# Kernel optimization log

Measured on AMD Instinct MI355X. Metric: run time of the kernel, lower is better.

Reference implementation:

```python
import jax, jax.numpy as jnp
import numpy as np

B, NM, NA, D = 16, 4000, 128, 128  # scenes, map nodes/scene, agents/scene, feature dim
DIST_TH = 7.0
BOX = 100.0


def _gn(x, g, b, eps=1e-5):
    # GroupNorm with 1 group over [N, C]: per-row normalization, biased variance, affine.
    mu = jnp.mean(x, axis=-1, keepdims=True)
    var = jnp.mean((x - mu) ** 2, axis=-1, keepdims=True)
    return (x - mu) * jax.lax.rsqrt(var + eps) * g + b


def _forward(feat, turn, control, intersect, agents, map_ctrs, agent_ctrs,
             meta_w, meta_g, meta_b,
             dist_w1, dist_b1, dist_w2, dist_g2, dist_b2,
             query_w, query_g, query_b,
             ctx_w1, ctx_g1, ctx_b1, ctx_w2,
             agt_w, norm_g, norm_b,
             lin_w, lin_g, lin_b,
             hi, wi):
    relu = jax.nn.relu
    # meta fuse: cat(feat, turn, control, intersect) -> Linear(n_map+4 -> n_map) + GN + ReLU
    x = jnp.concatenate([feat, turn, control[:, None], intersect[:, None]], axis=1)
    x = relu(_gn(x @ meta_w.T, meta_g, meta_b))
    for i in range(2):  # two Att layers with distinct weights
        res = x
        d = map_ctrs[hi] - agent_ctrs[wi]                         # [E, 2]
        d = relu(d @ dist_w1[i].T + dist_b1[i])                   # [E, D]
        d = relu(_gn(d @ dist_w2[i].T, dist_g2[i], dist_b2[i]))
        q = relu(_gn(x[hi] @ query_w[i].T, query_g[i], query_b[i]))
        c = jnp.concatenate([d, q, agents[wi]], axis=1)           # [E, 3D]
        c = relu(_gn(c @ ctx_w1[i].T, ctx_g1[i], ctx_b1[i]))
        c = c @ ctx_w2[i].T                                       # [E, D]
        x = x @ agt_w[i].T                                        # [N, D]
        x = x.at[hi].add(c)                                       # index_add_ scatter
        x = relu(_gn(x, norm_g[i], norm_b[i]))
        x = _gn(x @ lin_w[i].T, lin_g[i], lin_b[i])               # Linear act=False
        x = relu(x + res)
    return x


def setup_inputs() -> dict:
    # edge list (hi: map node, wi: agent) built exactly like Att's per-scene dist<=th nonzero
    rng = np.random.default_rng(0)
    mc = rng.uniform(0.0, BOX, (B, NM, 2)).astype(np.float32)
    ac = rng.uniform(0.0, BOX, (B, NA, 2)).astype(np.float32)
    dist = np.sqrt(((mc[:, :, None, :] - ac[:, None, :, :]) ** 2).sum(-1))
    bb, h, w = np.nonzero(dist <= DIST_TH)
    hi = jnp.asarray((bb * NM + h).astype(np.int32))
    wi = jnp.asarray((bb * NA + w).astype(np.int32))

    key = jax.random.key(0)
    ks = jax.random.split(key, 20)
    s = 0.02
    nrm = lambda k, shape: jax.random.normal(k, shape, jnp.float32) * s
    return {
        "feat": jax.random.normal(ks[0], (B * NM, D), jnp.float32),
        "turn": jax.random.normal(ks[1], (B * NM, 2), jnp.float32),
        "control": jax.random.uniform(ks[2], (B * NM,), jnp.float32),
        "intersect": jax.random.uniform(ks[3], (B * NM,), jnp.float32),
        "agents": jax.random.normal(ks[4], (B * NA, D), jnp.float32),
        "map_ctrs": jnp.asarray(mc.reshape(-1, 2)),
        "agent_ctrs": jnp.asarray(ac.reshape(-1, 2)),
        "meta_w": nrm(ks[5], (D, D + 4)),
        "meta_g": jnp.ones((D,), jnp.float32),
        "meta_b": jnp.zeros((D,), jnp.float32),
        "dist_w1": nrm(ks[6], (2, D, 2)),
        "dist_b1": nrm(ks[7], (2, D)),
        "dist_w2": nrm(ks[8], (2, D, D)),
        "dist_g2": jnp.ones((2, D), jnp.float32),
        "dist_b2": jnp.zeros((2, D), jnp.float32),
        "query_w": nrm(ks[9], (2, D, D)),
        "query_g": jnp.ones((2, D), jnp.float32),
        "query_b": jnp.zeros((2, D), jnp.float32),
        "ctx_w1": nrm(ks[10], (2, D, 3 * D)),
        "ctx_g1": jnp.ones((2, D), jnp.float32),
        "ctx_b1": jnp.zeros((2, D), jnp.float32),
        "ctx_w2": nrm(ks[11], (2, D, D)),
        "agt_w": nrm(ks[12], (2, D, D)),
        "norm_g": jnp.ones((2, D), jnp.float32),
        "norm_b": jnp.zeros((2, D), jnp.float32),
        "lin_w": nrm(ks[13], (2, D, D)),
        "lin_g": jnp.ones((2, D), jnp.float32),
        "lin_b": jnp.zeros((2, D), jnp.float32),
        "hi": hi,
        "wi": wi,
    }


def reference(feat, turn, control, intersect, agents, map_ctrs, agent_ctrs,
              meta_w, meta_g, meta_b,
              dist_w1, dist_b1, dist_w2, dist_g2, dist_b2,
              query_w, query_g, query_b,
              ctx_w1, ctx_g1, ctx_b1, ctx_w2,
              agt_w, norm_g, norm_b,
              lin_w, lin_g, lin_b,
              hi, wi):
    return _forward(feat, turn, control, intersect, agents, map_ctrs, agent_ctrs,
                    meta_w, meta_g, meta_b,
                    dist_w1, dist_b1, dist_w2, dist_g2, dist_b2,
                    query_w, query_g, query_b,
                    ctx_w1, ctx_g1, ctx_b1, ctx_w2,
                    agt_w, norm_g, norm_b,
                    lin_w, lin_g, lin_b,
                    hi, wi)
```

## Files before the change

kernel.cpp:

```cpp
#include <hip/hip_runtime.h>


typedef __attribute__((ext_vector_type(8))) short short8v;
typedef __attribute__((ext_vector_type(4))) float f32x4;

#define NXCD 8

__device__ __forceinline__ unsigned short f2b(float f) {
    union { float f; unsigned u; } v; v.f = f;
    return (unsigned short)((v.u + 0x7fffu + ((v.u >> 16) & 1u)) >> 16);
}
__device__ __forceinline__ unsigned pk2(float a, float b) {
    return (unsigned)f2b(a) | ((unsigned)f2b(b) << 16);
}
__device__ __forceinline__ float bflo(unsigned u) { return __uint_as_float(u << 16); }
__device__ __forceinline__ float bfhi(unsigned u) { return __uint_as_float(u & 0xffff0000u); }

union U4S8 { unsigned u[4]; short8v v; };

__device__ __forceinline__ void bar_lds() {
    __builtin_amdgcn_sched_barrier(0);
    asm volatile("s_waitcnt lgkmcnt(0)" ::: "memory");
    __builtin_amdgcn_s_barrier();
    __builtin_amdgcn_sched_barrier(0);
}

template<int NV>
__device__ __forceinline__ void sload(short8v (&v)[NV], const unsigned short* __restrict__ src,
                                      int t) {
#pragma unroll
    for (int i = 0; i < NV; i++) v[i] = *(const short8v*)(src + (size_t)i * 2048 + t * 8);
}
template<int NV>
__device__ __forceinline__ void swrite(unsigned short* dst, const short8v (&v)[NV], int t) {
#pragma unroll
    for (int i = 0; i < NV; i++) *(short8v*)(dst + i * 2048 + t * 8) = v[i];
}

template<int NK>
__device__ __forceinline__ void wgemm_lds(const unsigned short* Wlds,
                                          const short8v* bf, f32x4 (&acc)[8], int l) {
#pragma unroll
    for (int mt = 0; mt < 8; mt++) {
        acc[mt] = (f32x4){0.f, 0.f, 0.f, 0.f};
#pragma unroll
        for (int kk = 0; kk < NK; kk++) {
            const short8v a = *(const short8v*)(Wlds + ((mt * NK + kk) * 64 + l) * 8);
            acc[mt] = __builtin_amdgcn_mfma_f32_16x16x32_bf16(a, bf[kk], acc[mt], 0, 0, 0);
        }
    }
}

__device__ __forceinline__ void gn_apply8(f32x4 (&acc)[8], const float* __restrict__ g,
                                          const float* __restrict__ b, int lg, bool relu) {
    float s = 0.f, s2 = 0.f;
#pragma unroll
    for (int mt = 0; mt < 8; mt++)
#pragma unroll
        for (int q = 0; q < 4; q++) { const float v = acc[mt][q]; s += v; s2 += v * v; }
    s += __shfl_xor(s, 16, 64); s2 += __shfl_xor(s2, 16, 64);
    s += __shfl_xor(s, 32, 64); s2 += __shfl_xor(s2, 32, 64);
    const float mu = s * (1.f / 128.f);
    const float rs = rsqrtf(s2 * (1.f / 128.f) - mu * mu + 1e-5f);
#pragma unroll
    for (int mt = 0; mt < 8; mt++) {
        const f32x4 g4 = *(const f32x4*)(g + mt * 16 + lg * 4);
        const f32x4 b4 = *(const f32x4*)(b + mt * 16 + lg * 4);
#pragma unroll
        for (int q = 0; q < 4; q++) {
            float y = (acc[mt][q] - mu) * rs * g4[q] + b4[q];
            acc[mt][q] = relu ? fmaxf(y, 0.f) : y;
        }
    }
}

__device__ __forceinline__ void pack_p(const f32x4 (&acc)[8], unsigned (&p)[8][2]) {
#pragma unroll
    for (int mt = 0; mt < 8; mt++) {
        p[mt][0] = pk2(acc[mt][0], acc[mt][1]);
        p[mt][1] = pk2(acc[mt][2], acc[mt][3]);
    }
}

__device__ __forceinline__ void lds_put(unsigned short* wslice, const unsigned (&p)[8][2],
                                        int lg, int col) {
#pragma unroll
    for (int mt = 0; mt < 8; mt++) {
        const unsigned long long v = (unsigned long long)p[mt][0] |
                                     ((unsigned long long)p[mt][1] << 32);
        *(unsigned long long*)((char*)wslice + ((col * 256 + mt * 32 + lg * 8) ^ ((col & 7) << 4))) = v;
    }
}
__device__ __forceinline__ void lds_wait() {
    asm volatile("s_waitcnt lgkmcnt(0)" ::: "memory");
    __builtin_amdgcn_sched_barrier(0);
}
__device__ __forceinline__ void lds_get(const unsigned short* wslice, int lg, int col,
                                        short8v* bf) {
#pragma unroll
    for (int kk = 0; kk < 4; kk++)
        bf[kk] = *(const short8v*)((const char*)wslice +
                 ((col * 256 + kk * 64 + lg * 16) ^ ((col & 7) << 4)));
}
__device__ __forceinline__ void relayout1(unsigned short* wslice, int lg, int col,
                                          f32x4 (&acc)[8], short8v* bf) {
    unsigned p[8][2];
    pack_p(acc, p); lds_put(wslice, p, lg, col); lds_wait(); lds_get(wslice, lg, col, bf);
}

__device__ __forceinline__ void load_bfrag_row(const float* __restrict__ src, int lg,
                                               short8v* bf) {
#pragma unroll
    for (int kk = 0; kk < 4; kk++) {
        const f32x4 a = *(const f32x4*)(src + kk * 32 + lg * 8);
        const f32x4 b = *(const f32x4*)(src + kk * 32 + lg * 8 + 4);
        U4S8 u;
        u.u[0] = pk2(a[0], a[1]); u.u[1] = pk2(a[2], a[3]);
        u.u[2] = pk2(b[0], b[1]); u.u[3] = pk2(b[2], b[3]);
        bf[kk] = u.v;
    }
}
__device__ __forceinline__ void store_rows(float* dst, const f32x4 (&acc)[8], int lg) {
#pragma unroll
    for (int mt = 0; mt < 8; mt++) *(f32x4*)(dst + mt * 16 + lg * 4) = acc[mt];
}
__device__ __forceinline__ void store_rows_bf16(unsigned short* dst, const f32x4 (&acc)[8], int lg) {
#pragma unroll
    for (int mt = 0; mt < 8; mt++) {
        uint2 u; u.x = pk2(acc[mt][0], acc[mt][1]); u.y = pk2(acc[mt][2], acc[mt][3]);
        *(uint2*)(dst + mt * 16 + lg * 4) = u;
    }
}
__device__ __forceinline__ void residual_add_bf16(f32x4 (&acc)[8],
                                                  const unsigned short* __restrict__ rp,
                                                  int lg, bool relu) {
#pragma unroll
    for (int mt = 0; mt < 8; mt++) {
        const uint2 u = *(const uint2*)(rp + mt * 16 + lg * 4);
        acc[mt][0] += bflo(u.x); acc[mt][1] += bfhi(u.x);
        acc[mt][2] += bflo(u.y); acc[mt][3] += bfhi(u.y);
        if (relu) {
#pragma unroll
            for (int q = 0; q < 4; q++) acc[mt][q] = fmaxf(acc[mt][q], 0.f);
        }
    }
}
__device__ __forceinline__ void gather_issue(const unsigned short* __restrict__ Qc,
                                             const unsigned short* __restrict__ Acp,
                                             int h, int w, int lg,
                                             uint2 (&qv)[8], uint2 (&av)[8]) {
    const int hl = (h < 0) ? 0 : h;
    const unsigned short* qp = Qc  + (size_t)hl * 128 + lg * 4;
    const unsigned short* ap = Acp + (size_t)w  * 128 + lg * 4;
#pragma unroll
    for (int mt = 0; mt < 8; mt++) {
        qv[mt] = *(const uint2*)(qp + mt * 16);
        av[mt] = *(const uint2*)(ap + mt * 16);
    }
}
__device__ __forceinline__ void gather_add(f32x4 (&acc)[8], const uint2 (&qv)[8],
                                           const uint2 (&av)[8]) {
#pragma unroll
    for (int mt = 0; mt < 8; mt++) {
        acc[mt][0] += bflo(qv[mt].x) + bflo(av[mt].x);
        acc[mt][1] += bfhi(qv[mt].x) + bfhi(av[mt].x);
        acc[mt][2] += bflo(qv[mt].y) + bflo(av[mt].y);
        acc[mt][3] += bfhi(qv[mt].y) + bfhi(av[mt].y);
    }
}
__device__ __forceinline__ void build_d1(const float* __restrict__ dw1,
                                         const float* __restrict__ db1,
                                         float dx, float dy, int lg, short8v* bf) {
#pragma unroll
    for (int kk = 0; kk < 4; kk++) {
        U4S8 u;
#pragma unroll
        for (int ii = 0; ii < 4; ii++) {
            const int c0 = kk * 32 + lg * 8 + ii * 2;
            const float2 wa = *(const float2*)(dw1 + 2 * c0);
            const float2 wb = *(const float2*)(dw1 + 2 * c0 + 2);
            const float2 bb = *(const float2*)(db1 + c0);
            u.u[ii] = pk2(fmaxf(fmaf(wa.x, dx, fmaf(wa.y, dy, bb.x)), 0.f),
                          fmaxf(fmaf(wb.x, dx, fmaf(wb.y, dy, bb.y)), 0.f));
        }
        bf[kk] = u.v;
    }
}

struct PrepJob { const float* src; int dst; int ld; int kmax; int nk; };
struct PrepJobs { PrepJob j[17]; };

__global__ __launch_bounds__(64) void prep_weights(PrepJobs P, unsigned short* __restrict__ pool) {
    const PrepJob J = P.j[blockIdx.y];
    const int f = blockIdx.x;
    if (f >= 8 * J.nk) return;
    const int l = threadIdx.x;
    const int n = (f / J.nk) * 16 + (l & 15);
    const int kb = (f % J.nk) * 32 + (l >> 4) * 8;
    float v[8];
#pragma unroll
    for (int i = 0; i < 8; i++) {
        const int k = kb + i;
        v[i] = (k < J.kmax) ? J.src[(size_t)n * J.ld + k] : 0.f;
    }
    U4S8 u;
#pragma unroll
    for (int i = 0; i < 4; i++) u.u[i] = pk2(v[2 * i], v[2 * i + 1]);
    *(short8v*)(pool + J.dst + ((size_t)f * 64 + l) * 8) = u.v;
}

__device__ __forceinline__ void agent_path(
    unsigned short* Wlds, int abid, int NA, const float* __restrict__ agents,
    const unsigned short* __restrict__ Wc1a, unsigned short* Ac,
    int t, int wid, int l, int lg, int col)
{
    short8v sv[8];
    sload<8>(sv, Wc1a, t);
    const int r = abid * 64 + wid * 16 + col;
    const int rc = min(r, NA - 1);
    short8v bf[4];
    load_bfrag_row(agents + (size_t)rc * 128, lg, bf);
    swrite<8>(Wlds, sv, t);
    bar_lds();
    f32x4 acc[8];
    wgemm_lds<4>(Wlds, bf, acc, l);
    if (r < NA) store_rows_bf16(Ac + (size_t)r * 128, acc, lg);
}

__global__ __launch_bounds__(256, 2) void meta_node(
    const int N, const int NA, const int gN,
    const float* __restrict__ feat, const float* __restrict__ turn,
    const float* __restrict__ ctrl, const float* __restrict__ inter,
    const float* __restrict__ agents,
    const unsigned short* __restrict__ Wm,
    const float* __restrict__ mg, const float* __restrict__ mb,
    const unsigned short* __restrict__ Wagt, const unsigned short* __restrict__ Wq,
    const float* __restrict__ qg, const float* __restrict__ qb,
    const unsigned short* __restrict__ Wc1q, const unsigned short* __restrict__ Wc1a,
    unsigned short* __restrict__ xA, float* __restrict__ xB,
    unsigned short* __restrict__ Qc, unsigned short* __restrict__ Ac)
{
    __shared__ unsigned short Wlds[20480];
    const int t = threadIdx.x, wid = t >> 6, l = t & 63, lg = l >> 4, col = l & 15;
    unsigned short* wslice = Wlds + wid * 2048;
    if (blockIdx.x >= gN) {
        agent_path(Wlds, blockIdx.x - gN, NA, agents, Wc1a, Ac, t, wid, l, lg, col);
        return;
    }
    const int r = blockIdx.x * 64 + wid * 16 + col;
    const int rc = min(r, N - 1);

    short8v s10[10];
    sload<10>(s10, Wm, t);
    short8v bf[5];
    load_bfrag_row(feat + (size_t)rc * 128, lg, bf);
    {
        U4S8 u; u.u[0] = 0; u.u[1] = 0; u.u[2] = 0; u.u[3] = 0;
        if (lg == 0) {
            const float2 tv = *(const float2*)(turn + (size_t)rc * 2);
            u.u[0] = pk2(tv.x, tv.y);
            u.u[1] = pk2(ctrl[rc], inter[rc]);
        }
        bf[4] = u.v;
    }
    swrite<10>(Wlds, s10, t);
    bar_lds();

    short8v s8[8];
    sload<8>(s8, Wagt, t);
    f32x4 acc[8];
    wgemm_lds<5>(Wlds, bf, acc, l);
    gn_apply8(acc, mg, mb, lg, true);
    if (r < N) store_rows_bf16(xA + (size_t)r * 128, acc, lg);
    bar_lds();
    short8v bx[4];
    relayout1(wslice, lg, col, acc, bx);
    bar_lds();
    swrite<8>(Wlds, s8, t);
    bar_lds();

    sload<8>(s8, Wq, t);
    wgemm_lds<4>(Wlds, bx, acc, l);
    if (r < N) store_rows(xB + (size_t)r * 128, acc, lg);
    bar_lds();
    swrite<8>(Wlds, s8, t);
    bar_lds();

    sload<8>(s8, Wc1q, t);
    wgemm_lds<4>(Wlds, bx, acc, l);
    gn_apply8(acc, qg, qb, lg, true);
    bar_lds();
    relayout1(wslice, lg, col, acc, bx);
    bar_lds();
    swrite<8>(Wlds, s8, t);
    bar_lds();

    wgemm_lds<4>(Wlds, bx, acc, l);
    if (r < N) store_rows_bf16(Qc + (size_t)r * 128, acc, lg);
}

__device__ __forceinline__ void post_load_gn(const float* xp,
                                             const float* __restrict__ ng,
                                             const float* __restrict__ nb,
                                             int lg, short8v* bf) {
    float v[4][8];
    float s = 0.f, s2 = 0.f;
#pragma unroll
    for (int kk = 0; kk < 4; kk++) {
        *(f32x4*)(v[kk])     = *(const f32x4*)(xp + kk * 32 + lg * 8);
        *(f32x4*)(v[kk] + 4) = *(const f32x4*)(xp + kk * 32 + lg * 8 + 4);
#pragma unroll
        for (int i = 0; i < 8; i++) { s += v[kk][i]; s2 += v[kk][i] * v[kk][i]; }
    }
    s += __shfl_xor(s, 16, 64); s2 += __shfl_xor(s2, 16, 64);
    s += __shfl_xor(s, 32, 64); s2 += __shfl_xor(s2, 32, 64);
    const float mu = s * (1.f / 128.f);
    const float rs = rsqrtf(s2 * (1.f / 128.f) - mu * mu + 1e-5f);
#pragma unroll
    for (int kk = 0; kk < 4; kk++) {
        float y[8];
#pragma unroll
        for (int i = 0; i < 8; i += 4) {
            const f32x4 g4 = *(const f32x4*)(ng + kk * 32 + lg * 8 + i);
            const f32x4 b4 = *(const f32x4*)(nb + kk * 32 + lg * 8 + i);
#pragma unroll
            for (int q = 0; q < 4; q++)
                y[i + q] = fmaxf((v[kk][i + q] - mu) * rs * g4[q] + b4[q], 0.f);
        }
        U4S8 u;
#pragma unroll
        for (int i = 0; i < 4; i++) u.u[i] = pk2(y[2 * i], y[2 * i + 1]);
        bf[kk] = u.v;
    }
}

__global__ __launch_bounds__(256, 2) void post_node(
    const int N, const int NA, const int gN,
    const float* __restrict__ ng, const float* __restrict__ nb,
    const unsigned short* __restrict__ Wlin,
    const float* __restrict__ lgam, const float* __restrict__ lbet,
    const float* __restrict__ agents, const unsigned short* __restrict__ Wc1a,
    const unsigned short* __restrict__ Wagt, const unsigned short* __restrict__ Wq,
    const float* __restrict__ qg, const float* __restrict__ qb,
    const unsigned short* __restrict__ Wc1q,
    unsigned short* xA, float* xB,
    unsigned short* __restrict__ Qc, unsigned short* __restrict__ Ac)
{
    __shared__ unsigned short Wlds[16384];
    const int t = threadIdx.x, wid = t >> 6, l = t & 63, lg = l >> 4, col = l & 15;
    unsigned short* wslice = Wlds + wid * 2048;
    if (blockIdx.x >= gN) {
        agent_path(Wlds, blockIdx.x - gN, NA, agents, Wc1a, Ac, t, wid, l, lg, col);
        return;
    }
    const int r = blockIdx.x * 64 + wid * 16 + col;
    const int rc = min(r, N - 1);

    short8v s8[8];
    sload<8>(s8, Wlin, t);
    short8v bf[4];
    post_load_gn(xB + (size_t)rc * 128, ng, nb, lg, bf);
    swrite<8>(Wlds, s8, t);
    bar_lds();

    sload<8>(s8, Wagt, t);
    f32x4 acc[8];
    wgemm_lds<4>(Wlds, bf, acc, l);
    gn_apply8(acc, lgam, lbet, lg, false);
    residual_add_bf16(acc, xA + (size_t)rc * 128, lg, true);
    if (r < N) store_rows_bf16(xA + (size_t)r * 128, acc, lg);
    bar_lds();
    short8v bx[4];
    relayout1(wslice, lg, col, acc, bx);
    bar_lds();
    swrite<8>(Wlds, s8, t);
    bar_lds();

    sload<8>(s8, Wq, t);
    wgemm_lds<4>(Wlds, bx, acc, l);
    if (r < N) store_rows(xB + (size_t)r * 128, acc, lg);
    bar_lds();
    swrite<8>(Wlds, s8, t);
    bar_lds();

    sload<8>(s8, Wc1q, t);
    wgemm_lds<4>(Wlds, bx, acc, l);
    gn_apply8(acc, qg, qb, lg, true);
    bar_lds();
    relayout1(wslice, lg, col, acc, bx);
    bar_lds();
    swrite<8>(Wlds, s8, t);
    bar_lds();

    wgemm_lds<4>(Wlds, bx, acc, l);
    if (r < N) store_rows_bf16(Qc + (size_t)r * 128, acc, lg);
}

__global__ __launch_bounds__(256, 2) void post_final(
    const int N,
    const float* __restrict__ xB,
    const float* __restrict__ ng, const float* __restrict__ nb,
    const unsigned short* __restrict__ Wlin,
    const float* __restrict__ lgam, const float* __restrict__ lbet,
    const unsigned short* __restrict__ res, float* __restrict__ out)
{
    __shared__ unsigned short Wlds[16384];
    const int t = threadIdx.x, wid = t >> 6, l = t & 63, lg = l >> 4, col = l & 15;
    const int r = blockIdx.x * 64 + wid * 16 + col;
    const int rc = min(r, N - 1);
    short8v s8[8];
    sload<8>(s8, Wlin, t);
    short8v bf[4];
    post_load_gn(xB + (size_t)rc * 128, ng, nb, lg, bf);
    swrite<8>(Wlds, s8, t);
    bar_lds();
    f32x4 acc[8];
    wgemm_lds<4>(Wlds, bf, acc, l);
    gn_apply8(acc, lgam, lbet, lg, false);
    residual_add_bf16(acc, res + (size_t)rc * 128, lg, true);
    if (r < N) store_rows(out + (size_t)r * 128, acc, lg);
}

__global__ __launch_bounds__(256, 2) void edge_mfma(
    const int E, const int nwg,
    const int* __restrict__ hi, const int* __restrict__ wi,
    const float* __restrict__ mc, const float* __restrict__ ac,
    const float* __restrict__ dw1, const float* __restrict__ db1,
    const unsigned short* __restrict__ Wd2, const float* __restrict__ dg2, const float* __restrict__ db2,
    const unsigned short* __restrict__ Wc1d, const float* __restrict__ cg1, const float* __restrict__ cb1,
    const unsigned short* __restrict__ Wc2,
    const unsigned short* __restrict__ Qc, const unsigned short* __restrict__ Acp,
    float* __restrict__ OUT)
{
    __shared__ unsigned short Wlds[16384];
    __shared__ int s_h[64];
    const int t = threadIdx.x, wid = t >> 6, l = t & 63, lg = l >> 4, col = l & 15;
    unsigned short* wslice = Wlds + wid * 2048;

    int bid;
    {
        const int orig = blockIdx.x;
        const int q = nwg / NXCD, r = nwg % NXCD;
        const int xcd = orig % NXCD, i = orig / NXCD;
        bid = (xcd < r ? xcd * (q + 1) : r * (q + 1) + (xcd - r) * q) + i;
    }
    const int eidx = bid * 64 + wid * 16 + col;

    short8v s8[8];
    sload<8>(s8, Wd2, t);

    int h = -1, w = 0;
    if (eidx < E) { h = hi[eidx]; w = wi[eidx]; }
    if (lg == 0) s_h[wid * 16 + col] = h;
    const int hl = (h < 0) ? 0 : h;
    const float2 mcv = *(const float2*)(mc + 2 * (size_t)hl);
    const float2 acv = *(const float2*)(ac + 2 * (size_t)w);
    const float dx = mcv.x - acv.x, dy = mcv.y - acv.y;

    uint2 qv[8], av[8];
    gather_issue(Qc, Acp, h, w, lg, qv, av);

    short8v bf[4];
    build_d1(dw1, db1, dx, dy, lg, bf);

    swrite<8>(Wlds, s8, t);
    bar_lds();

    sload<8>(s8, Wc1d, t);
    f32x4 acc[8];
    wgemm_lds<4>(Wlds, bf, acc, l);
    gn_apply8(acc, dg2, db2, lg, true);
    bar_lds();
    relayout1(wslice, lg, col, acc, bf);
    bar_lds();
    swrite<8>(Wlds, s8, t);
    bar_lds();

    sload<8>(s8, Wc2, t);
    wgemm_lds<4>(Wlds, bf, acc, l);
    gather_add(acc, qv, av);
    gn_apply8(acc, cg1, cb1, lg, true);
    bar_lds();
    relayout1(wslice, lg, col, acc, bf);
    bar_lds();
    swrite<8>(Wlds, s8, t);
    bar_lds();

    wgemm_lds<4>(Wlds, bf, acc, l);
    bar_lds();
    unsigned p[8][2];
    pack_p(acc, p); lds_put(wslice, p, lg, col); lds_wait();

#pragma unroll
    for (int pass = 0; pass < 2; pass++) {
        const int c = pass * 64 + l;
        float pend = 0.f; int ph = -1;
#pragma unroll
        for (int e = 0; e < 16; e++) {
            const int he = s_h[wid * 16 + e];
            const unsigned short uv = *(const unsigned short*)((const char*)wslice +
                                      ((e * 256 + c * 2) ^ ((e & 7) << 4)));
            const float v = __uint_as_float((unsigned)uv << 16);
            if (he == ph) pend += v;
            else {
                if (ph >= 0) atomicAdd(&OUT[(size_t)ph * 128 + c], pend);
                ph = he; pend = v;
            }
        }
        if (ph >= 0) atomicAdd(&OUT[(size_t)ph * 128 + c], pend);
    }
}

extern "C" void kernel_launch(void* const* d_in, const int* in_sizes, int n_in,
                              void* d_out, int out_size, void* d_ws, size_t ws_size,
                              hipStream_t stream)
{
    const float* feat    = (const float*)d_in[0];
    const float* turn    = (const float*)d_in[1];
    const float* ctrl    = (const float*)d_in[2];
    const float* inter   = (const float*)d_in[3];
    const float* agents  = (const float*)d_in[4];
    const float* mc      = (const float*)d_in[5];
    const float* ac      = (const float*)d_in[6];
    const float* meta_w  = (const float*)d_in[7];
    const float* meta_g  = (const float*)d_in[8];
    const float* meta_b  = (const float*)d_in[9];
    const float* dist_w1 = (const float*)d_in[10];
    const float* dist_b1 = (const float*)d_in[11];
    const float* dist_w2 = (const float*)d_in[12];
    const float* dist_g2 = (const float*)d_in[13];
    const float* dist_b2 = (const float*)d_in[14];
    const float* query_w = (const float*)d_in[15];
    const float* query_g = (const float*)d_in[16];
    const float* query_b = (const float*)d_in[17];
    const float* ctx_w1  = (const float*)d_in[18];
    const float* ctx_g1  = (const float*)d_in[19];
    const float* ctx_b1  = (const float*)d_in[20];
    const float* ctx_w2  = (const float*)d_in[21];
    const float* agt_w   = (const float*)d_in[22];
    const float* norm_g  = (const float*)d_in[23];
    const float* norm_b  = (const float*)d_in[24];
    const float* lin_w   = (const float*)d_in[25];
    const float* lin_g   = (const float*)d_in[26];
    const float* lin_b   = (const float*)d_in[27];
    const int*   hi      = (const int*)d_in[28];
    const int*   wi      = (const int*)d_in[29];

    const int E  = in_sizes[28];
    const int N  = in_sizes[0] / 128;
    const int NA = in_sizes[4] / 128;

    unsigned short* xA = (unsigned short*)d_ws;
    float* xB = (float*)(xA + (size_t)N * 128);
    unsigned short* pool = (unsigned short*)(xB + (size_t)N * 128);

    const int FR128  = 8 * 4 * 64 * 8;
    const int FRMETA = 8 * 5 * 64 * 8;
    const int POOL_ELEMS = FRMETA + 16 * FR128;

    unsigned short* Ac = pool + POOL_ELEMS;
    unsigned short* Qc = (unsigned short*)d_out;

    PrepJobs P;
    P.j[0] = { meta_w, 0, 132, 132, 5 };
    for (int i = 0; i < 2; i++) {
        const int b = FRMETA + i * 8 * FR128;
        P.j[1 + i * 8 + 0] = { query_w + (size_t)i * 16384, b + 0 * FR128, 128, 128, 4 };
        P.j[1 + i * 8 + 1] = { agt_w   + (size_t)i * 16384, b + 1 * FR128, 128, 128, 4 };
        P.j[1 + i * 8 + 2] = { dist_w2 + (size_t)i * 16384, b + 2 * FR128, 128, 128, 4 };
        P.j[1 + i * 8 + 3] = { ctx_w1  + (size_t)i * 49152,       b + 3 * FR128, 384, 128, 4 };
        P.j[1 + i * 8 + 4] = { ctx_w1  + (size_t)i * 49152 + 128, b + 4 * FR128, 384, 128, 4 };
        P.j[1 + i * 8 + 5] = { ctx_w2  + (size_t)i * 16384, b + 5 * FR128, 128, 128, 4 };
        P.j[1 + i * 8 + 6] = { lin_w   + (size_t)i * 16384, b + 6 * FR128, 128, 128, 4 };
        P.j[1 + i * 8 + 7] = { ctx_w1  + (size_t)i * 49152 + 256, b + 7 * FR128, 384, 128, 4 };
    }
    prep_weights<<<dim3(40, 17), 64, 0, stream>>>(P, pool);

    const int gN = (N + 63) / 64;
    const int gA = (NA + 63) / 64;
    const int gE = (E + 63) / 64;

    const unsigned short* W0 = pool + FRMETA;
    const unsigned short* W1 = pool + FRMETA + 8 * FR128;

    meta_node<<<gN + gA, 256, 0, stream>>>(
        N, NA, gN, feat, turn, ctrl, inter, agents,
        pool, meta_g, meta_b,
        W0 + 1 * FR128, W0 + 0 * FR128, query_g, query_b,
        W0 + 4 * FR128, W0 + 7 * FR128,
        xA, xB, Qc, Ac);

    edge_mfma<<<gE, 256, 0, stream>>>(
        E, gE, hi, wi, mc, ac,
        dist_w1, dist_b1,
        W0 + 2 * FR128, dist_g2, dist_b2,
        W0 + 3 * FR128, ctx_g1, ctx_b1,
        W0 + 5 * FR128, Qc, Ac, xB);

    post_node<<<gN + gA, 256, 0, stream>>>(
        N, NA, gN,
        norm_g, norm_b, W0 + 6 * FR128, lin_g, lin_b,
        agents, W1 + 7 * FR128,
        W1 + 1 * FR128, W1 + 0 * FR128, query_g + 128, query_b + 128,
        W1 + 4 * FR128,
        xA, xB, Qc, Ac);

    edge_mfma<<<gE, 256, 0, stream>>>(
        E, gE, hi, wi, mc, ac,
        dist_w1 + 256, dist_b1 + 128,
        W1 + 2 * FR128, dist_g2 + 128, dist_b2 + 128,
        W1 + 3 * FR128, ctx_g1 + 128, ctx_b1 + 128,
        W1 + 5 * FR128, Qc, Ac, xB);

    post_final<<<gN, 256, 0, stream>>>(
        N, xB, norm_g + 128, norm_b + 128,
        W1 + 6 * FR128, lin_g + 128, lin_b + 128, xA, (float*)d_out);
}
```

Before: 191.7 us.

## Preload all edge weights into LDS once with 512-thread edge blocks

The edge kernel now uses 512-thread blocks covering 128 edges, loads all three 128x128 weight matrices into a single larger LDS buffer up front, and drops the intermediate barriers and weight swaps between the three GEMMs. Scatter target indices are re-read from global memory with nontemporal loads instead of being kept in shared memory. The aim is to amortise weight staging over more edges and cut barrier stalls, at the cost of higher LDS use (about 128 KB per block) and one block per CU. A leftover dead shuffle loop is also present.

```diff
diff --git a/kernel.cpp b/kernel.cpp
--- a/kernel.cpp
+++ b/kernel.cpp
@@ -25,16 +25,16 @@
     __builtin_amdgcn_sched_barrier(0);
 }
 
-template<int NV>
+template<int NV, int NT>
 __device__ __forceinline__ void sload(short8v (&v)[NV], const unsigned short* __restrict__ src,
                                       int t) {
 #pragma unroll
-    for (int i = 0; i < NV; i++) v[i] = *(const short8v*)(src + (size_t)i * 2048 + t * 8);
-}
-template<int NV>
+    for (int i = 0; i < NV; i++) v[i] = *(const short8v*)(src + (size_t)i * (NT * 8) + t * 8);
+}
+template<int NV, int NT>
 __device__ __forceinline__ void swrite(unsigned short* dst, const short8v (&v)[NV], int t) {
 #pragma unroll
-    for (int i = 0; i < NV; i++) *(short8v*)(dst + i * 2048 + t * 8) = v[i];
+    for (int i = 0; i < NV; i++) *(short8v*)(dst + i * (NT * 8) + t * 8) = v[i];
 }
 
 template<int NK>
@@ -215,12 +215,12 @@
     int t, int wid, int l, int lg, int col)
 {
     short8v sv[8];
-    sload<8>(sv, Wc1a, t);
+    sload<8, 256>(sv, Wc1a, t);
     const int r = abid * 64 + wid * 16 + col;
     const int rc = min(r, NA - 1);
     short8v bf[4];
     load_bfrag_row(agents + (size_t)rc * 128, lg, bf);
-    swrite<8>(Wlds, sv, t);
+    swrite<8, 256>(Wlds, sv, t);
     bar_lds();
     f32x4 acc[8];
     wgemm_lds<4>(Wlds, bf, acc, l);
@@ -251,7 +251,7 @@
     const int rc = min(r, N - 1);
 
     short8v s10[10];
-    sload<10>(s10, Wm, t);
+    sload<10, 256>(s10, Wm, t);
     short8v bf[5];
     load_bfrag_row(feat + (size_t)rc * 128, lg, bf);
     {
@@ -263,11 +263,11 @@
         }
         bf[4] = u.v;
     }
-    swrite<10>(Wlds, s10, t);
+    swrite<10, 256>(Wlds, s10, t);
     bar_lds();
 
     short8v s8[8];
-    sload<8>(s8, Wagt, t);
+    sload<8, 256>(s8, Wagt, t);
     f32x4 acc[8];
     wgemm_lds<5>(Wlds, bf, acc, l);
     gn_apply8(acc, mg, mb, lg, true);
@@ -276,23 +276,23 @@
     short8v bx[4];
     relayout1(wslice, lg, col, acc, bx);
     bar_lds();
-    swrite<8>(Wlds, s8, t);
-    bar_lds();
-
-    sload<8>(s8, Wq, t);
+    swrite<8, 256>(Wlds, s8, t);
+    bar_lds();
+
+    sload<8, 256>(s8, Wq, t);
     wgemm_lds<4>(Wlds, bx, acc, l);
     if (r < N) store_rows(xB + (size_t)r * 128, acc, lg);
     bar_lds();
-    swrite<8>(Wlds, s8, t);
-    bar_lds();
-
-    sload<8>(s8, Wc1q, t);
+    swrite<8, 256>(Wlds, s8, t);
+    bar_lds();
+
+    sload<8, 256>(s8, Wc1q, t);
     wgemm_lds<4>(Wlds, bx, acc, l);
     gn_apply8(acc, qg, qb, lg, true);
     bar_lds();
     relayout1(wslice, lg, col, acc, bx);
     bar_lds();
-    swrite<8>(Wlds, s8, t);
+    swrite<8, 256>(Wlds, s8, t);
     bar_lds();
 
     wgemm_lds<4>(Wlds, bx, acc, l);
@@ -357,13 +357,13 @@
     const int rc = min(r, N - 1);
 
     short8v s8[8];
-    sload<8>(s8, Wlin, t);
+    sload<8, 256>(s8, Wlin, t);
     short8v bf[4];
     post_load_gn(xB + (size_t)rc * 128, ng, nb, lg, bf);
-    swrite<8>(Wlds, s8, t);
-    bar_lds();
-
-    sload<8>(s8, Wagt, t);
+    swrite<8, 256>(Wlds, s8, t);
+    bar_lds();
+
+    sload<8, 256>(s8, Wagt, t);
     f32x4 acc[8];
     wgemm_lds<4>(Wlds, bf, acc, l);
     gn_apply8(acc, lgam, lbet, lg, false);
@@ -373,23 +373,23 @@
     short8v bx[4];
     relayout1(wslice, lg, col, acc, bx);
     bar_lds();
-    swrite<8>(Wlds, s8, t);
-    bar_lds();
-
-    sload<8>(s8, Wq, t);
+    swrite<8, 256>(Wlds, s8, t);
+    bar_lds();
+
+    sload<8, 256>(s8, Wq, t);
     wgemm_lds<4>(Wlds, bx, acc, l);
     if (r < N) store_rows(xB + (size_t)r * 128, acc, lg);
     bar_lds();
-    swrite<8>(Wlds, s8, t);
-    bar_lds();
-
-    sload<8>(s8, Wc1q, t);
+    swrite<8, 256>(Wlds, s8, t);
+    bar_lds();
+
+    sload<8, 256>(s8, Wc1q, t);
     wgemm_lds<4>(Wlds, bx, acc, l);
     gn_apply8(acc, qg, qb, lg, true);
     bar_lds();
     relayout1(wslice, lg, col, acc, bx);
     bar_lds();
-    swrite<8>(Wlds, s8, t);
+    swrite<8, 256>(Wlds, s8, t);
     bar_lds();
 
     wgemm_lds<4>(Wlds, bx, acc, l);
@@ -409,10 +409,10 @@
     const int r = blockIdx.x * 64 + wid * 16 + col;
     const int rc = min(r, N - 1);
     short8v s8[8];
-    sload<8>(s8, Wlin, t);
+    sload<8, 256>(s8, Wlin, t);
     short8v bf[4];
     post_load_gn(xB + (size_t)rc * 128, ng, nb, lg, bf);
-    swrite<8>(Wlds, s8, t);
+    swrite<8, 256>(Wlds, s8, t);
     bar_lds();
     f32x4 acc[8];
     wgemm_lds<4>(Wlds, bf, acc, l);
@@ -421,7 +421,7 @@
     if (r < N) store_rows(out + (size_t)r * 128, acc, lg);
 }
 
-__global__ __launch_bounds__(256, 2) void edge_mfma(
+__global__ __launch_bounds__(512, 1) void edge_mfma(
     const int E, const int nwg,
     const int* __restrict__ hi, const int* __restrict__ wi,
     const float* __restrict__ mc, const float* __restrict__ ac,
@@ -432,10 +432,9 @@
     const unsigned short* __restrict__ Qc, const unsigned short* __restrict__ Acp,
     float* __restrict__ OUT)
 {
-    __shared__ unsigned short Wlds[16384];
-    __shared__ int s_h[64];
+    __shared__ unsigned short Wall[49152 + 8 * 2048];
     const int t = threadIdx.x, wid = t >> 6, l = t & 63, lg = l >> 4, col = l & 15;
-    unsigned short* wslice = Wlds + wid * 2048;
+    unsigned short* wslice = Wall + 49152 + wid * 2048;
 
     int bid;
     {
@@ -444,14 +443,15 @@
         const int xcd = orig % NXCD, i = orig / NXCD;
         bid = (xcd < r ? xcd * (q + 1) : r * (q + 1) + (xcd - r) * q) + i;
     }
-    const int eidx = bid * 64 + wid * 16 + col;
-
-    short8v s8[8];
-    sload<8>(s8, Wd2, t);
+    const int eidx = bid * 128 + wid * 16 + col;
+
+    short8v sd[4], sc1[4], sc2[4];
+    sload<4, 512>(sd,  Wd2,  t);
+    sload<4, 512>(sc1, Wc1d, t);
+    sload<4, 512>(sc2, Wc2,  t);
 
     int h = -1, w = 0;
     if (eidx < E) { h = hi[eidx]; w = wi[eidx]; }
-    if (lg == 0) s_h[wid * 16 + col] = h;
     const int hl = (h < 0) ? 0 : h;
     const float2 mcv = *(const float2*)(mc + 2 * (size_t)hl);
     const float2 acv = *(const float2*)(ac + 2 * (size_t)w);
@@ -463,41 +463,49 @@
     short8v bf[4];
     build_d1(dw1, db1, dx, dy, lg, bf);
 
-    swrite<8>(Wlds, s8, t);
-    bar_lds();
-
-    sload<8>(s8, Wc1d, t);
+    swrite<4, 512>(Wall,         sd,  t);
+    swrite<4, 512>(Wall + 16384, sc1, t);
+    swrite<4, 512>(Wall + 32768, sc2, t);
+    bar_lds();
+
     f32x4 acc[8];
-    wgemm_lds<4>(Wlds, bf, acc, l);
+    wgemm_lds<4>(Wall, bf, acc, l);
     gn_apply8(acc, dg2, db2, lg, true);
-    bar_lds();
     relayout1(wslice, lg, col, acc, bf);
-    bar_lds();
-    swrite<8>(Wlds, s8, t);
-    bar_lds();
-
-    sload<8>(s8, Wc2, t);
-    wgemm_lds<4>(Wlds, bf, acc, l);
+
+    wgemm_lds<4>(Wall + 16384, bf, acc, l);
     gather_add(acc, qv, av);
     gn_apply8(acc, cg1, cb1, lg, true);
-    bar_lds();
     relayout1(wslice, lg, col, acc, bf);
-    bar_lds();
-    swrite<8>(Wlds, s8, t);
-    bar_lds();
-
-    wgemm_lds<4>(Wlds, bf, acc, l);
-    bar_lds();
+
+    wgemm_lds<4>(Wall + 32768, bf, acc, l);
     unsigned p[8][2];
     pack_p(acc, p); lds_put(wslice, p, lg, col); lds_wait();
 
+    const int ebase16 = bid * 128 + wid * 16;
 #pragma unroll
     for (int pass = 0; pass < 2; pass++) {
         const int c = pass * 64 + l;
         float pend = 0.f; int ph = -1;
 #pragma unroll
         for (int e = 0; e < 16; e++) {
-            const int he = s_h[wid * 16 + e];
+            const int ei = ebase16 + e;
+            const int he = (ei < E) ? __shfl(h, e * 4, 64) : -1;
+            (void)ei; (void)he;
+        }
+        (void)c; (void)pend; (void)ph;
+    }
+    {
+    }
+#pragma unroll
+    for (int pass = 0; pass < 2; pass++) {
+        const int c = pass * 64 + l;
+        float pend = 0.f; int ph = -1;
+#pragma unroll
+        for (int e = 0; e < 16; e++) {
+            const int ei = ebase16 + e;
+            int he = -1;
+            if (ei < E) he = __builtin_nontemporal_load(hi + ei);
             const unsigned short uv = *(const unsigned short*)((const char*)wslice +
                                       ((e * 256 + c * 2) ^ ((e & 7) << 4)));
             const float v = __uint_as_float((unsigned)uv << 16);
@@ -578,7 +586,7 @@
 
     const int gN = (N + 63) / 64;
     const int gA = (NA + 63) / 64;
-    const int gE = (E + 63) / 64;
+    const int gE = (E + 127) / 128;
 
     const unsigned short* W0 = pool + FRMETA;
     const unsigned short* W1 = pool + FRMETA + 8 * FR128;
@@ -590,7 +598,7 @@
         W0 + 4 * FR128, W0 + 7 * FR128,
         xA, xB, Qc, Ac);
 
-    edge_mfma<<<gE, 256, 0, stream>>>(
+    edge_mfma<<<gE, 512, 0, stream>>>(
         E, gE, hi, wi, mc, ac,
         dist_w1, dist_b1,
         W0 + 2 * FR128, dist_g2, dist_b2,
@@ -605,7 +613,7 @@
         W1 + 4 * FR128,
         xA, xB, Qc, Ac);
 
-    edge_mfma<<<gE, 256, 0, stream>>>(
+    edge_mfma<<<gE, 512, 0, stream>>>(
         E, gE, hi, wi, mc, ac,
         dist_w1 + 256, dist_b1 + 128,
         W1 + 2 * FR128, dist_g2 + 128, dist_b2 + 128,
```

New measurement: 286.5 us. 49.4% more time.

## Move ctx_w2 GEMM from edges to nodes by scattering pre-projection context

Applied to the files above, without the earlier changes.

Linearity of ctx_w2 lets the edge kernel scatter-add the GN+ReLU context output into a separate fp32 buffer S, so the per-edge 128x128 GEMM is dropped. The node kernels then run one GEMM per node (S @ Wc2) and add it to the agt_w projection. This cuts GEMM work from E rows to N rows and removes one weight load per edge block. It costs an extra zero pass over S, an extra node-side GEMM stage, and different rounding, since S is now rounded to bf16 before the matmul.

```diff
diff --git a/kernel.cpp b/kernel.cpp
--- a/kernel.cpp
+++ b/kernel.cpp
@@ -123,6 +123,20 @@
 __device__ __forceinline__ void store_rows(float* dst, const f32x4 (&acc)[8], int lg) {
 #pragma unroll
     for (int mt = 0; mt < 8; mt++) *(f32x4*)(dst + mt * 16 + lg * 4) = acc[mt];
+}
+__device__ __forceinline__ void zero_rows(float* dst, int lg) {
+    const f32x4 z = (f32x4){0.f, 0.f, 0.f, 0.f};
+#pragma unroll
+    for (int mt = 0; mt < 8; mt++) *(f32x4*)(dst + mt * 16 + lg * 4) = z;
+}
+__device__ __forceinline__ void add_rows_f32(f32x4 (&acc)[8], const float* __restrict__ rp,
+                                             int lg) {
+#pragma unroll
+    for (int mt = 0; mt < 8; mt++) {
+        const f32x4 r4 = *(const f32x4*)(rp + mt * 16 + lg * 4);
+#pragma unroll
+        for (int q = 0; q < 4; q++) acc[mt][q] += r4[q];
+    }
 }
 __device__ __forceinline__ void store_rows_bf16(unsigned short* dst, const f32x4 (&acc)[8], int lg) {
 #pragma unroll
@@ -237,7 +251,7 @@
     const unsigned short* __restrict__ Wagt, const unsigned short* __restrict__ Wq,
     const float* __restrict__ qg, const float* __restrict__ qb,
     const unsigned short* __restrict__ Wc1q, const unsigned short* __restrict__ Wc1a,
-    unsigned short* __restrict__ xA, float* __restrict__ xB,
+    unsigned short* __restrict__ xA, float* __restrict__ xB, float* __restrict__ S,
     unsigned short* __restrict__ Qc, unsigned short* __restrict__ Ac)
 {
     __shared__ unsigned short Wlds[20480];
@@ -281,7 +295,10 @@
 
     sload<8>(s8, Wq, t);
     wgemm_lds<4>(Wlds, bx, acc, l);
-    if (r < N) store_rows(xB + (size_t)r * 128, acc, lg);
+    if (r < N) {
+        store_rows(xB + (size_t)r * 128, acc, lg);
+        zero_rows(S + (size_t)r * 128, lg);
+    }
     bar_lds();
     swrite<8>(Wlds, s8, t);
     bar_lds();
@@ -297,45 +314,11 @@
 
     wgemm_lds<4>(Wlds, bx, acc, l);
     if (r < N) store_rows_bf16(Qc + (size_t)r * 128, acc, lg);
-}
-
-__device__ __forceinline__ void post_load_gn(const float* xp,
-                                             const float* __restrict__ ng,
-                                             const float* __restrict__ nb,
-                                             int lg, short8v* bf) {
-    float v[4][8];
-    float s = 0.f, s2 = 0.f;
-#pragma unroll
-    for (int kk = 0; kk < 4; kk++) {
-        *(f32x4*)(v[kk])     = *(const f32x4*)(xp + kk * 32 + lg * 8);
-        *(f32x4*)(v[kk] + 4) = *(const f32x4*)(xp + kk * 32 + lg * 8 + 4);
-#pragma unroll
-        for (int i = 0; i < 8; i++) { s += v[kk][i]; s2 += v[kk][i] * v[kk][i]; }
-    }
-    s += __shfl_xor(s, 16, 64); s2 += __shfl_xor(s2, 16, 64);
-    s += __shfl_xor(s, 32, 64); s2 += __shfl_xor(s2, 32, 64);
-    const float mu = s * (1.f / 128.f);
-    const float rs = rsqrtf(s2 * (1.f / 128.f) - mu * mu + 1e-5f);
-#pragma unroll
-    for (int kk = 0; kk < 4; kk++) {
-        float y[8];
-#pragma unroll
-        for (int i = 0; i < 8; i += 4) {
-            const f32x4 g4 = *(const f32x4*)(ng + kk * 32 + lg * 8 + i);
-            const f32x4 b4 = *(const f32x4*)(nb + kk * 32 + lg * 8 + i);
-#pragma unroll
-            for (int q = 0; q < 4; q++)
-                y[i + q] = fmaxf((v[kk][i + q] - mu) * rs * g4[q] + b4[q], 0.f);
-        }
-        U4S8 u;
-#pragma unroll
-        for (int i = 0; i < 4; i++) u.u[i] = pk2(y[2 * i], y[2 * i + 1]);
-        bf[kk] = u.v;
-    }
 }
 
 __global__ __launch_bounds__(256, 2) void post_node(
     const int N, const int NA, const int gN,
+    const unsigned short* __restrict__ Wc2,
     const float* __restrict__ ng, const float* __restrict__ nb,
     const unsigned short* __restrict__ Wlin,
     const float* __restrict__ lgam, const float* __restrict__ lbet,
@@ -343,7 +326,7 @@
     const unsigned short* __restrict__ Wagt, const unsigned short* __restrict__ Wq,
     const float* __restrict__ qg, const float* __restrict__ qb,
     const unsigned short* __restrict__ Wc1q,
-    unsigned short* xA, float* xB,
+    unsigned short* xA, float* xB, float* S,
     unsigned short* __restrict__ Qc, unsigned short* __restrict__ Ac)
 {
     __shared__ unsigned short Wlds[16384];
@@ -357,20 +340,30 @@
     const int rc = min(r, N - 1);
 
     short8v s8[8];
+    sload<8>(s8, Wc2, t);
+    short8v bf[4];
+    load_bfrag_row(S + (size_t)rc * 128, lg, bf);
+    swrite<8>(Wlds, s8, t);
+    bar_lds();
+
     sload<8>(s8, Wlin, t);
-    short8v bf[4];
-    post_load_gn(xB + (size_t)rc * 128, ng, nb, lg, bf);
-    swrite<8>(Wlds, s8, t);
-    bar_lds();
-
-    sload<8>(s8, Wagt, t);
     f32x4 acc[8];
     wgemm_lds<4>(Wlds, bf, acc, l);
+    add_rows_f32(acc, xB + (size_t)rc * 128, lg);
+    gn_apply8(acc, ng, nb, lg, true);
+    bar_lds();
+    short8v bx[4];
+    relayout1(wslice, lg, col, acc, bx);
+    bar_lds();
+    swrite<8>(Wlds, s8, t);
+    bar_lds();
+
+    sload<8>(s8, Wagt, t);
+    wgemm_lds<4>(Wlds, bx, acc, l);
     gn_apply8(acc, lgam, lbet, lg, false);
     residual_add_bf16(acc, xA + (size_t)rc * 128, lg, true);
     if (r < N) store_rows_bf16(xA + (size_t)r * 128, acc, lg);
     bar_lds();
-    short8v bx[4];
     relayout1(wslice, lg, col, acc, bx);
     bar_lds();
     swrite<8>(Wlds, s8, t);
@@ -378,7 +371,10 @@
 
     sload<8>(s8, Wq, t);
     wgemm_lds<4>(Wlds, bx, acc, l);
-    if (r < N) store_rows(xB + (size_t)r * 128, acc, lg);
+    if (r < N) {
+        store_rows(xB + (size_t)r * 128, acc, lg);
+        zero_rows(S + (size_t)r * 128, lg);
+    }
     bar_lds();
     swrite<8>(Wlds, s8, t);
     bar_lds();
@@ -398,7 +394,8 @@
 
 __global__ __launch_bounds__(256, 2) void post_final(
     const int N,
-    const float* __restrict__ xB,
+    const unsigned short* __restrict__ Wc2,
+    const float* __restrict__ xB, const float* __restrict__ S,
     const float* __restrict__ ng, const float* __restrict__ nb,
     const unsigned short* __restrict__ Wlin,
     const float* __restrict__ lgam, const float* __restrict__ lbet,
@@ -406,16 +403,30 @@
 {
     __shared__ unsigned short Wlds[16384];
     const int t = threadIdx.x, wid = t >> 6, l = t & 63, lg = l >> 4, col = l & 15;
+    unsigned short* wslice = Wlds + wid * 2048;
     const int r = blockIdx.x * 64 + wid * 16 + col;
     const int rc = min(r, N - 1);
+
     short8v s8[8];
+    sload<8>(s8, Wc2, t);
+    short8v bf[4];
+    load_bfrag_row(S + (size_t)rc * 128, lg, bf);
+    swrite<8>(Wlds, s8, t);
+    bar_lds();
+
     sload<8>(s8, Wlin, t);
-    short8v bf[4];
-    post_load_gn(xB + (size_t)rc * 128, ng, nb, lg, bf);
-    swrite<8>(Wlds, s8, t);
-    bar_lds();
     f32x4 acc[8];
     wgemm_lds<4>(Wlds, bf, acc, l);
+    add_rows_f32(acc, xB + (size_t)rc * 128, lg);
+    gn_apply8(acc, ng, nb, lg, true);
+    bar_lds();
+    short8v bx[4];
+    relayout1(wslice, lg, col, acc, bx);
+    bar_lds();
+    swrite<8>(Wlds, s8, t);
+    bar_lds();
+
+    wgemm_lds<4>(Wlds, bx, acc, l);
     gn_apply8(acc, lgam, lbet, lg, false);
     residual_add_bf16(acc, res + (size_t)rc * 128, lg, true);
     if (r < N) store_rows(out + (size_t)r * 128, acc, lg);
@@ -428,9 +439,8 @@
     const float* __restrict__ dw1, const float* __restrict__ db1,
     const unsigned short* __restrict__ Wd2, const float* __restrict__ dg2, const float* __restrict__ db2,
     const unsigned short* __restrict__ Wc1d, const float* __restrict__ cg1, const float* __restrict__ cb1,
-    const unsigned short* __restrict__ Wc2,
     const unsigned short* __restrict__ Qc, const unsigned short* __restrict__ Acp,
-    float* __restrict__ OUT)
+    float* __restrict__ S)
 {
     __shared__ unsigned short Wlds[16384];
     __shared__ int s_h[64];
@@ -476,17 +486,9 @@
     swrite<8>(Wlds, s8, t);
     bar_lds();
 
-    sload<8>(s8, Wc2, t);
     wgemm_lds<4>(Wlds, bf, acc, l);
     gather_add(acc, qv, av);
     gn_apply8(acc, cg1, cb1, lg, true);
-    bar_lds();
-    relayout1(wslice, lg, col, acc, bf);
-    bar_lds();
-    swrite<8>(Wlds, s8, t);
-    bar_lds();
-
-    wgemm_lds<4>(Wlds, bf, acc, l);
     bar_lds();
     unsigned p[8][2];
     pack_p(acc, p); lds_put(wslice, p, lg, col); lds_wait();
@@ -503,11 +505,11 @@
             const float v = __uint_as_float((unsigned)uv << 16);
             if (he == ph) pend += v;
             else {
-                if (ph >= 0) atomicAdd(&OUT[(size_t)ph * 128 + c], pend);
+                if (ph >= 0) atomicAdd(&S[(size_t)ph * 128 + c], pend);
                 ph = he; pend = v;
             }
         }
-        if (ph >= 0) atomicAdd(&OUT[(size_t)ph * 128 + c], pend);
+        if (ph >= 0) atomicAdd(&S[(size_t)ph * 128 + c], pend);
     }
 }
 
@@ -552,7 +554,8 @@
 
     unsigned short* xA = (unsigned short*)d_ws;
     float* xB = (float*)(xA + (size_t)N * 128);
-    unsigned short* pool = (unsigned short*)(xB + (size_t)N * 128);
+    float* S  = xB + (size_t)N * 128;
+    unsigned short* pool = (unsigned short*)(S + (size_t)N * 128);
 
     const int FR128  = 8 * 4 * 64 * 8;
     const int FRMETA = 8 * 5 * 64 * 8;
@@ -588,31 +591,33 @@
         pool, meta_g, meta_b,
         W0 + 1 * FR128, W0 + 0 * FR128, query_g, query_b,
         W0 + 4 * FR128, W0 + 7 * FR128,
-        xA, xB, Qc, Ac);
+        xA, xB, S, Qc, Ac);
 
     edge_mfma<<<gE, 256, 0, stream>>>(
         E, gE, hi, wi, mc, ac,
         dist_w1, dist_b1,
         W0 + 2 * FR128, dist_g2, dist_b2,
         W0 + 3 * FR128, ctx_g1, ctx_b1,
-        W0 + 5 * FR128, Qc, Ac, xB);
+        Qc, Ac, S);
 
     post_node<<<gN + gA, 256, 0, stream>>>(
         N, NA, gN,
+        W0 + 5 * FR128,
         norm_g, norm_b, W0 + 6 * FR128, lin_g, lin_b,
         agents, W1 + 7 * FR128,
         W1 + 1 * FR128, W1 + 0 * FR128, query_g + 128, query_b + 128,
         W1 + 4 * FR128,
-        xA, xB, Qc, Ac);
+        xA, xB, S, Qc, Ac);
 
     edge_mfma<<<gE, 256, 0, stream>>>(
         E, gE, hi, wi, mc, ac,
         dist_w1 + 256, dist_b1 + 128,
         W1 + 2 * FR128, dist_g2 + 128, dist_b2 + 128,
         W1 + 3 * FR128, ctx_g1 + 128, ctx_b1 + 128,
-        W1 + 5 * FR128, Qc, Ac, xB);
+        Qc, Ac, S);
 
     post_final<<<gN, 256, 0, stream>>>(
-        N, xB, norm_g + 128, norm_b + 128,
+        N, W1 + 5 * FR128, xB, S,
+        norm_g + 128, norm_b + 128,
         W1 + 6 * FR128, lin_g + 128, lin_b + 128, xA, (float*)d_out);
 }
```

After: 217.5 us. +13.4%, slower.
